# Performance work log

Measured on AMD Instinct MI355X. Metric: run time of the kernel, lower is better.

The kernel has to match this reference:

```python
import jax, jax.numpy as jnp
import numpy as np

B, N, C = 8192, 4, 768          # B = batch*tokens, N = n_streams, C = dim
HID = 4 * C                      # FFN hidden
EPS_RMS = 1.1920929e-7           # torch.finfo(float32).eps (nn.RMSNorm default eps=None)
EPS_SK = 1e-6                    # sinkhorn eps
SK_ITERS = 20
ALPHA = 0.01


def setup_inputs() -> dict:
    key = jax.random.key(0)
    ks = jax.random.split(key, 7)
    w = lambda k, shape: (jax.random.normal(k, shape, jnp.float32) * 0.02)
    return {
        "x": jax.random.normal(ks[0], (B, N, C), jnp.float32),
        "norm_w": jnp.ones((N * C,), jnp.float32),
        "w_pre": w(ks[1], (N, N * C)),
        "b_pre": jnp.zeros((N,), jnp.float32),
        "w_post": w(ks[2], (N, N * C)),
        "b_post": jnp.zeros((N,), jnp.float32),
        "w_res": w(ks[3], (N * N, N * C)),
        "b_res": jnp.zeros((N * N,), jnp.float32),
        "alpha_pre": jnp.array(ALPHA, jnp.float32),
        "alpha_post": jnp.array(ALPHA, jnp.float32),
        "alpha_res": jnp.array(ALPHA, jnp.float32),
        "w1": w(ks[4], (HID, C)),   # torch Linear weight layout [out, in]
        "b1": jnp.zeros((HID,), jnp.float32),
        "w2": w(ks[5], (C, HID)),
        "b2": jnp.zeros((C,), jnp.float32),
    }


def sinkhorn_knopp(logits):
    # logits: [B, n, n] -> doubly-stochastic matrix via 20 row/col normalizations
    M0 = jnp.exp(logits)

    def body(_, M):
        M = M / (M.sum(axis=-1, keepdims=True) + EPS_SK)
        M = M / (M.sum(axis=-2, keepdims=True) + EPS_SK)
        return M

    return jax.lax.fori_loop(0, SK_ITERS, body, M0)


def reference(x, norm_w, w_pre, b_pre, w_post, b_post, w_res, b_res,
              alpha_pre, alpha_post, alpha_res, w1, b1, w2, b2):
    b, n, c = x.shape
    x_flat = x.reshape(b, n * c)
    # RMSNorm over flattened streams
    x_norm = x_flat * jax.lax.rsqrt(jnp.mean(x_flat * x_flat, axis=-1, keepdims=True) + EPS_RMS) * norm_w
    # gate logits
    pre = alpha_pre * (x_norm @ w_pre.T) + b_pre            # [B, n]
    post = alpha_post * (x_norm @ w_post.T) + b_post        # [B, n]
    res_logits = (alpha_res * (x_norm @ w_res.T) + b_res).reshape(b, n, n)
    H_pre = jax.nn.sigmoid(pre)
    H_post = 2.0 * jax.nn.sigmoid(post)
    H_res = sinkhorn_knopp(res_logits)                      # [B, n, n]
    # pre-gate + stream mixing
    x_pre = x * H_pre[..., None]                            # [B, n, C]
    x_streams = jnp.einsum('bij,bjc->bic', H_res, x_pre)
    # fn = FFN applied on [B*n, C]
    h = jax.nn.gelu(x_streams.reshape(b * n, c) @ w1.T + b1, approximate=False)
    y = (h @ w2.T + b2).reshape(b, n, c)
    y = y * H_post[..., None]
    # residual mixed by the same DSM
    res = jnp.einsum('bij,bjc->bic', H_res, x)
    return res + y
```

## Files before the change

### kernel.cpp

```cpp
#include <hip/hip_runtime.h>

#define EPS_RMS 1.1920929e-7f
#define EPS_SK  1e-6f

typedef __bf16 bf16;
typedef __bf16 bf16x4 __attribute__((ext_vector_type(4)));
typedef __bf16 bf16x8 __attribute__((ext_vector_type(8)));
typedef float  f32x4  __attribute__((ext_vector_type(4)));

typedef __attribute__((address_space(3))) void lds_void;
typedef __attribute__((address_space(1))) void glb_void;

__device__ __forceinline__ void async_copy16(void* lds_dst, const void* gsrc) {
  __builtin_amdgcn_global_load_lds((glb_void*)gsrc, (lds_void*)lds_dst, 16, 0, 0);
}

template<int N> __device__ __forceinline__ void wait_vmcnt() {
  if constexpr (N == 6)      asm volatile("s_waitcnt vmcnt(6)" ::: "memory");
  else if constexpr (N == 5) asm volatile("s_waitcnt vmcnt(5)" ::: "memory");
  else                       asm volatile("s_waitcnt vmcnt(0)" ::: "memory");
}
__device__ __forceinline__ void lgkm0_fence() {
  asm volatile("s_waitcnt lgkmcnt(0)" ::: "memory");
  __builtin_amdgcn_sched_barrier(0);
}

__device__ __forceinline__ void xcd_swizzle(int& bx, int& by) {
  const int gx = gridDim.x, nwg = gx * gridDim.y;
  const int flat = blockIdx.y * gx + blockIdx.x;
  const int q = nwg >> 3, r = nwg & 7;
  const int xcd = flat & 7, i = flat >> 3;
  const int lin = (xcd < r ? xcd * (q + 1) : r * (q + 1) + (xcd - r) * q) + i;
  bx = lin % gx;
  by = lin / gx;
}

__global__ __launch_bounds__(256) void convert_w_kernel(
    const float* __restrict__ w1, const float* __restrict__ w2,
    bf16* __restrict__ w1b, bf16* __restrict__ w2b) {
  size_t i = ((size_t)blockIdx.x * 256 + threadIdx.x) * 4;
  f32x4 a = *(const f32x4*)(w1 + i);
  f32x4 b = *(const f32x4*)(w2 + i);
  bf16x4 ab, bb;
#pragma unroll
  for (int q = 0; q < 4; ++q) { ab[q] = (bf16)a[q]; bb[q] = (bf16)b[q]; }
  *(bf16x4*)(w1b + i) = ab;
  *(bf16x4*)(w2b + i) = bb;
}

__global__ __launch_bounds__(256) void prep_wnb_kernel(
    const float* __restrict__ w_pre, const float* __restrict__ w_post,
    const float* __restrict__ w_res, const float* __restrict__ norm_w,
    bf16* __restrict__ wnb) {
  const int i = (blockIdx.x * 256 + threadIdx.x) * 4;
  const int j = i / 3072, k = i - j * 3072;
  f32x4 wv;
  if (j < 24) {
    const float* src = j < 4 ? (w_pre + j * 3072)
                     : (j < 8 ? (w_post + (j - 4) * 3072) : (w_res + (j - 8) * 3072));
    const f32x4 nv = *(const f32x4*)(norm_w + k);
    wv = *(const f32x4*)(src + k);
    wv = wv * nv;
  } else {
    wv = f32x4{0.f, 0.f, 0.f, 0.f};
  }
  bf16x4 o;
#pragma unroll
  for (int q = 0; q < 4; ++q) o[q] = (bf16)wv[q];
  *(bf16x4*)(wnb + i) = o;
}

__global__ __launch_bounds__(256) void gates_kernel(
    const float* __restrict__ x, const bf16* __restrict__ wnb,
    const float* __restrict__ b_pre, const float* __restrict__ b_post,
    const float* __restrict__ b_res,
    const float* __restrict__ alpha_pre, const float* __restrict__ alpha_post,
    const float* __restrict__ alpha_res, float* __restrict__ gates) {
  const int t = threadIdx.x, wv = t >> 6, l = t & 63;
  const int r0 = blockIdx.x * 16;
  __shared__ float buf[4][16][32];
  __shared__ float bsq[4][16];

  f32x4 acc[2] = {};
  float sq = 0.f;
  const int kbase = wv * 768;
  const size_t arow = (size_t)(r0 + (l & 15)) * 3072;
  const int koff = (l >> 4) * 8;
#pragma unroll 1
  for (int ks = 0; ks < 24; ++ks) {
    const int k0 = kbase + ks * 32 + koff;
    const f32x4 a0 = *(const f32x4*)(x + arow + k0);
    const f32x4 a1 = *(const f32x4*)(x + arow + k0 + 4);
    sq += a0[0]*a0[0] + a0[1]*a0[1] + a0[2]*a0[2] + a0[3]*a0[3]
        + a1[0]*a1[0] + a1[1]*a1[1] + a1[2]*a1[2] + a1[3]*a1[3];
    bf16x8 af;
#pragma unroll
    for (int e = 0; e < 4; ++e) { af[e] = (bf16)a0[e]; af[4 + e] = (bf16)a1[e]; }
#pragma unroll
    for (int nf = 0; nf < 2; ++nf) {
      const bf16x8 bn = *(const bf16x8*)(wnb + (size_t)(nf * 16 + (l & 15)) * 3072 + k0);
      acc[nf] = __builtin_amdgcn_mfma_f32_16x16x32_bf16(af, bn, acc[nf], 0, 0, 0);
    }
  }
  sq += __shfl_xor(sq, 16);
  sq += __shfl_xor(sq, 32);
#pragma unroll
  for (int nf = 0; nf < 2; ++nf)
#pragma unroll
    for (int j = 0; j < 4; ++j)
      buf[wv][(l >> 4) * 4 + j][nf * 16 + (l & 15)] = acc[nf][j];
  if (l < 16) bsq[wv][l] = sq;
  __syncthreads();

  if (t < 16) {
    const int r = t;
    float dv[24];
#pragma unroll
    for (int j = 0; j < 24; ++j)
      dv[j] = buf[0][r][j] + buf[1][r][j] + buf[2][r][j] + buf[3][r][j];
    const float ssq = bsq[0][r] + bsq[1][r] + bsq[2][r] + bsq[3][r];
    const float rms = rsqrtf(ssq * (1.f / 3072.f) + EPS_RMS);
    const float ap = alpha_pre[0], apo = alpha_post[0], ar = alpha_res[0];
    float* g = gates + (size_t)(r0 + r) * 24;
    float M[16];
#pragma unroll
    for (int j = 0; j < 4; ++j) {
      const float p = ap * rms * dv[j] + b_pre[j];
      g[j] = 1.f / (1.f + __expf(-p));
      const float q = apo * rms * dv[4 + j] + b_post[j];
      g[4 + j] = 2.f / (1.f + __expf(-q));
    }
#pragma unroll
    for (int j = 0; j < 16; ++j) M[j] = __expf(ar * rms * dv[8 + j] + b_res[j]);
    for (int it = 0; it < 20; ++it) {
#pragma unroll
      for (int i = 0; i < 4; ++i) {
        const float s = M[i * 4] + M[i * 4 + 1] + M[i * 4 + 2] + M[i * 4 + 3] + EPS_SK;
        const float ri = __fdividef(1.f, s);
#pragma unroll
        for (int j = 0; j < 4; ++j) M[i * 4 + j] *= ri;
      }
#pragma unroll
      for (int j = 0; j < 4; ++j) {
        const float s = M[j] + M[4 + j] + M[8 + j] + M[12 + j] + EPS_SK;
        const float ri = __fdividef(1.f, s);
#pragma unroll
        for (int i = 0; i < 4; ++i) M[i * 4 + j] *= ri;
      }
    }
#pragma unroll
    for (int j = 0; j < 16; ++j) g[8 + j] = M[j];
  }
}

__global__ __launch_bounds__(256) void mix_kernel(
    const float* __restrict__ x, const float* __restrict__ gates,
    bf16* __restrict__ xs, bf16* __restrict__ resb) {
  const int t = threadIdx.x;
  const int b = blockIdx.x * 4 + (t >> 6);
  const int lane = t & 63;
  const float* g = gates + (size_t)b * 24;
  float mr[4][4], mp[4][4];
#pragma unroll
  for (int i = 0; i < 4; ++i)
#pragma unroll
    for (int j = 0; j < 4; ++j) {
      mr[i][j] = g[8 + i * 4 + j];
      mp[i][j] = mr[i][j] * g[j];
    }
#pragma unroll
  for (int cc = 0; cc < 3; ++cc) {
    const int c4 = lane + cc * 64;
    f32x4 xj[4];
#pragma unroll
    for (int j = 0; j < 4; ++j)
      xj[j] = *(const f32x4*)(x + (size_t)(b * 4 + j) * 768 + c4 * 4);
#pragma unroll
    for (int i = 0; i < 4; ++i) {
      f32x4 vr = mr[i][0] * xj[0] + mr[i][1] * xj[1] + mr[i][2] * xj[2] + mr[i][3] * xj[3];
      f32x4 vs = mp[i][0] * xj[0] + mp[i][1] * xj[1] + mp[i][2] * xj[2] + mp[i][3] * xj[3];
      bf16x4 ro, so;
#pragma unroll
      for (int qq = 0; qq < 4; ++qq) { ro[qq] = (bf16)vr[qq]; so[qq] = (bf16)vs[qq]; }
      *(bf16x4*)(resb + (size_t)(b * 4 + i) * 768 + c4 * 4) = ro;
      *(bf16x4*)(xs   + (size_t)(b * 4 + i) * 768 + c4 * 4) = so;
    }
  }
}

__device__ __forceinline__ void stage_block(
    const bf16* __restrict__ src, const int rowBase, const int K, const int k0,
    char* ldsBuf, const int blk, const int t) {
  const int r = t >> 3;
  const int c = (t & 7) ^ (r & 7);
  async_copy16(ldsBuf + blk * 8192 + t * 16,
               src + (size_t)(rowBase + blk * 64 + r) * K + k0 + c * 8);
}

template<int NB>
__device__ __forceinline__ void gemm256_core(
    const bf16* __restrict__ A, const bf16* __restrict__ B, const int K,
    const int tM, const int tN, char* AL, char* BL, f32x4 (&acc)[8][NB]) {
  constexpr int BBUF = NB * 8192;
  constexpr int NB1 = 2, NB2 = NB - 2;
  const int t = threadIdx.x, l = t & 63, w = t >> 6;
  const int wr = w >> 2, wc = w & 3;
  const int NT = K >> 6;
  const int arow = wr * 128 + (l & 15);
  const int brow = wc * (NB * 16) + (l & 15);
  const int cb = l >> 4;

  auto frag = [&](const char* base, int row, int ks) -> bf16x8 {
    const int c = ks * 4 + cb;
    return *(const bf16x8*)(base + row * 128 + ((c ^ (row & 7)) << 4));
  };

#pragma unroll
  for (int b = 0; b < 4; ++b) stage_block(A, tM, K, 0, AL, b, t);
#pragma unroll
  for (int b = 0; b < NB; ++b) stage_block(B, tN, K, 0, BL, b, t);
  stage_block(A, tM, K, 64, AL + 32768, 0, t);
  stage_block(A, tM, K, 64, AL + 32768, 2, t);
#pragma unroll
  for (int b = 0; b < NB; ++b) stage_block(B, tN, K, 64, BL + BBUF, b, t);
  wait_vmcnt<NB + 2>();
  __builtin_amdgcn_s_barrier();

  for (int T = 0; T < NT; ++T) {
    char* Ab = AL + (T & 1) * 32768;
    char* Bb = BL + (T & 1) * BBUF;
    char* An = AL + ((T + 1) & 1) * 32768;
    const int k1 = (T + 1) << 6, k2 = (T + 2) << 6;
    const bool s1 = (T + 1 < NT), s2 = (T + 2 < NT);
    bf16x8 af[4][2], b0[NB1][2], b1[NB2][2];

#pragma unroll
    for (int ks = 0; ks < 2; ++ks) {
#pragma unroll
      for (int ni = 0; ni < NB1; ++ni) b0[ni][ks] = frag(Bb, brow + ni * 16, ks);
#pragma unroll
      for (int mi = 0; mi < 4; ++mi) af[mi][ks] = frag(Ab, arow + mi * 16, ks);
    }
    __builtin_amdgcn_s_barrier();
    if (s1) { stage_block(A, tM, K, k1, An, 1, t); stage_block(A, tM, K, k1, An, 3, t); }
    lgkm0_fence();
    __builtin_amdgcn_s_setprio(1);
#pragma unroll
    for (int ks = 0; ks < 2; ++ks)
#pragma unroll
      for (int mi = 0; mi < 4; ++mi)
#pragma unroll
        for (int ni = 0; ni < NB1; ++ni)
          acc[mi][ni] = __builtin_amdgcn_mfma_f32_16x16x32_bf16(af[mi][ks], b0[ni][ks], acc[mi][ni], 0, 0, 0);
    __builtin_amdgcn_s_setprio(0);

#pragma unroll
    for (int ks = 0; ks < 2; ++ks)
#pragma unroll
      for (int ni = 0; ni < NB2; ++ni) b1[ni][ks] = frag(Bb, brow + (NB1 + ni) * 16, ks);
    __builtin_amdgcn_s_barrier();
    if (s2) { stage_block(A, tM, K, k2, Ab, 0, t); stage_block(A, tM, K, k2, Ab, 2, t); }
    lgkm0_fence();
    __builtin_amdgcn_s_setprio(1);
#pragma unroll
    for (int ks = 0; ks < 2; ++ks)
#pragma unroll
      for (int mi = 0; mi < 4; ++mi)
#pragma unroll
        for (int ni = 0; ni < NB2; ++ni)
          acc[mi][NB1 + ni] = __builtin_amdgcn_mfma_f32_16x16x32_bf16(af[mi][ks], b1[ni][ks], acc[mi][NB1 + ni], 0, 0, 0);
    __builtin_amdgcn_s_setprio(0);

#pragma unroll
    for (int ks = 0; ks < 2; ++ks)
#pragma unroll
      for (int mi = 0; mi < 4; ++mi) af[mi][ks] = frag(Ab, arow + (4 + mi) * 16, ks);
    __builtin_amdgcn_s_barrier();
    if (s2) { stage_block(B, tN, K, k2, Bb, 0, t); stage_block(B, tN, K, k2, Bb, 1, t); }
    lgkm0_fence();
    __builtin_amdgcn_s_setprio(1);
#pragma unroll
    for (int ks = 0; ks < 2; ++ks)
#pragma unroll
      for (int mi = 0; mi < 4; ++mi)
#pragma unroll
        for (int ni = 0; ni < NB1; ++ni)
          acc[4 + mi][ni] = __builtin_amdgcn_mfma_f32_16x16x32_bf16(af[mi][ks], b0[ni][ks], acc[4 + mi][ni], 0, 0, 0);
    __builtin_amdgcn_s_setprio(0);

    __builtin_amdgcn_s_barrier();
    if (s2) {
#pragma unroll
      for (int b = 2; b < NB; ++b) stage_block(B, tN, K, k2, Bb, b, t);
    }
    if (T < NT - 2)       wait_vmcnt<NB + 2>();
    else if (T == NT - 2) wait_vmcnt<0>();
    __builtin_amdgcn_s_setprio(1);
#pragma unroll
    for (int ks = 0; ks < 2; ++ks)
#pragma unroll
      for (int mi = 0; mi < 4; ++mi)
#pragma unroll
        for (int ni = 0; ni < NB2; ++ni)
          acc[4 + mi][NB1 + ni] = __builtin_amdgcn_mfma_f32_16x16x32_bf16(af[mi][ks], b1[ni][ks], acc[4 + mi][NB1 + ni], 0, 0, 0);
    __builtin_amdgcn_s_setprio(0);
  }
}

__global__ __launch_bounds__(512, 1) void ffn1_kernel(
    const bf16* __restrict__ xs, const bf16* __restrict__ w1b,
    const float* __restrict__ b1, bf16* __restrict__ h) {
  __shared__ __align__(16) char AL[2 * 32768];
  __shared__ __align__(16) char BL[2 * 32768];
  int bx, by; xcd_swizzle(bx, by);
  const int tM = by * 256, tN = bx * 256;
  f32x4 acc[8][4] = {};
  gemm256_core<4>(xs, w1b, 768, tM, tN, AL, BL, acc);

  const int t = threadIdx.x, l = t & 63;
  const int w = t >> 6, wr = w >> 2, wc = w & 3;
  float bias[4];
#pragma unroll
  for (int ni = 0; ni < 4; ++ni) bias[ni] = b1[tN + wc * 64 + ni * 16 + (l & 15)];
#pragma unroll
  for (int mi = 0; mi < 8; ++mi)
#pragma unroll
    for (int j = 0; j < 4; ++j) {
      const int m = tM + wr * 128 + mi * 16 + (l >> 4) * 4 + j;
#pragma unroll
      for (int ni = 0; ni < 4; ++ni) {
        const int n = tN + wc * 64 + ni * 16 + (l & 15);
        const float v = acc[mi][ni][j] + bias[ni];
        const float y2 = 1.5957691216f * (v + 0.044715f * v * v * v);
        const float g = __fdividef(v, 1.f + __expf(-y2));
        h[(size_t)m * 3072 + n] = (bf16)g;
      }
    }
}

__global__ __launch_bounds__(512, 1) void ffn2_kernel(
    const bf16* __restrict__ h, const bf16* __restrict__ w2b,
    const float* __restrict__ b2, const float* __restrict__ gates,
    const bf16* __restrict__ resb, float* __restrict__ outp, const int m0) {
  __shared__ __align__(16) char AL[2 * 32768];
  __shared__ __align__(16) char BL[2 * 24576];
  int bx, by; xcd_swizzle(bx, by);
  const int tM = by * 256, tN = bx * 192;
  f32x4 acc[8][3] = {};
  gemm256_core<3>(h, w2b, 3072, tM, tN, AL, BL, acc);

  const int t = threadIdx.x, l = t & 63;
  const int w = t >> 6, wr = w >> 2, wc = w & 3;
  float bias[3];
#pragma unroll
  for (int ni = 0; ni < 3; ++ni) bias[ni] = b2[tN + wc * 48 + ni * 16 + (l & 15)];
#pragma unroll
  for (int mi = 0; mi < 8; ++mi)
#pragma unroll
    for (int j = 0; j < 4; ++j) {
      const int mL = tM + wr * 128 + mi * 16 + (l >> 4) * 4 + j;
      const int mG = m0 + mL;
      const float hp = gates[(size_t)(mG >> 2) * 24 + 4 + (mG & 3)];
#pragma unroll
      for (int ni = 0; ni < 3; ++ni) {
        const int n = tN + wc * 48 + ni * 16 + (l & 15);
        const size_t o = (size_t)mG * 768 + n;
        outp[o] = (float)resb[o] + (acc[mi][ni][j] + bias[ni]) * hp;
      }
    }
}

extern "C" void kernel_launch(void* const* d_in, const int* in_sizes, int n_in,
                              void* d_out, int out_size, void* d_ws, size_t ws_size,
                              hipStream_t stream) {
  (void)in_sizes; (void)n_in; (void)out_size;
  const float* x         = (const float*)d_in[0];
  const float* norm_w    = (const float*)d_in[1];
  const float* w_pre     = (const float*)d_in[2];
  const float* b_pre     = (const float*)d_in[3];
  const float* w_post    = (const float*)d_in[4];
  const float* b_post    = (const float*)d_in[5];
  const float* w_res     = (const float*)d_in[6];
  const float* b_res     = (const float*)d_in[7];
  const float* alpha_pre = (const float*)d_in[8];
  const float* alpha_post= (const float*)d_in[9];
  const float* alpha_res = (const float*)d_in[10];
  const float* w1        = (const float*)d_in[11];
  const float* b1        = (const float*)d_in[12];
  const float* w2        = (const float*)d_in[13];
  const float* b2        = (const float*)d_in[14];
  float* outp = (float*)d_out;

  char* ws = (char*)d_ws;
  float* gates = (float*)ws;
  bf16*  w1b   = (bf16*)(ws + 786432);
  bf16*  w2b   = (bf16*)(ws + 5505024);
  bf16*  xs    = (bf16*)(ws + 10223616);
  bf16*  resb  = (bf16*)(ws + 60555264);
  bf16*  wnb   = (bf16*)(ws + 110886912);
  bf16*  h     = (bf16*)(ws + 111083520);

  size_t avail = ws_size > 111083520 ? ws_size - 111083520 : 0;
  long hrows = (long)(avail / (3072 * 2));
  hrows = (hrows / 256) * 256;
  if (hrows > 32768) hrows = 32768;
  if (hrows < 256) hrows = 256;

  convert_w_kernel<<<dim3(2304), dim3(256), 0, stream>>>(w1, w2, w1b, w2b);
  prep_wnb_kernel<<<dim3(96), dim3(256), 0, stream>>>(w_pre, w_post, w_res, norm_w, wnb);
  gates_kernel<<<dim3(512), dim3(256), 0, stream>>>(
      x, wnb, b_pre, b_post, b_res, alpha_pre, alpha_post, alpha_res, gates);
  mix_kernel<<<dim3(2048), dim3(256), 0, stream>>>(x, gates, xs, resb);

  for (long mo = 0; mo < 32768; mo += hrows) {
    const long mm = (32768 - mo) < hrows ? (32768 - mo) : hrows;
    ffn1_kernel<<<dim3(12, (unsigned)(mm / 256)), dim3(512), 0, stream>>>(
        xs + mo * 768, w1b, b1, h);
    ffn2_kernel<<<dim3(4, (unsigned)(mm / 256)), dim3(512), 0, stream>>>(
        h, w2b, b2, gates, resb, outp, (int)mo);
  }
}
```

Measured before the change: 484.3 us.

## Fuse stream mixing into gates kernel and simplify GEMM inner pipeline

Merges the separate mix kernel into the gates kernel. The sinkhorn matrix and pre-gate go through shared memory and the same block writes xs and resb, so one launch and the gates round-trip disappear. The x rows are re-read while likely still in cache. The GEMM core is also restructured from four B-fragment phases into two half-M phases, with all B fragments loaded up front and all next-tile staging issued at one point. This raises register pressure for B fragments and reduces the interleaving of loads with MFMA.

```diff
diff --git a/kernel.cpp b/kernel.cpp
--- a/kernel.cpp
+++ b/kernel.cpp
@@ -75,11 +75,13 @@
     const float* __restrict__ b_pre, const float* __restrict__ b_post,
     const float* __restrict__ b_res,
     const float* __restrict__ alpha_pre, const float* __restrict__ alpha_post,
-    const float* __restrict__ alpha_res, float* __restrict__ gates) {
+    const float* __restrict__ alpha_res, float* __restrict__ gates,
+    bf16* __restrict__ xs, bf16* __restrict__ resb) {
   const int t = threadIdx.x, wv = t >> 6, l = t & 63;
   const int r0 = blockIdx.x * 16;
   __shared__ float buf[4][16][32];
   __shared__ float bsq[4][16];
+  __shared__ float gm[16][20];
 
   f32x4 acc[2] = {};
   float sq = 0.f;
@@ -123,10 +125,12 @@
     const float ap = alpha_pre[0], apo = alpha_post[0], ar = alpha_res[0];
     float* g = gates + (size_t)(r0 + r) * 24;
     float M[16];
+    float hp[4];
 #pragma unroll
     for (int j = 0; j < 4; ++j) {
       const float p = ap * rms * dv[j] + b_pre[j];
-      g[j] = 1.f / (1.f + __expf(-p));
+      hp[j] = 1.f / (1.f + __expf(-p));
+      g[j] = hp[j];
       const float q = apo * rms * dv[4 + j] + b_post[j];
       g[4 + j] = 2.f / (1.f + __expf(-q));
     }
@@ -149,41 +153,38 @@
       }
     }
 #pragma unroll
-    for (int j = 0; j < 16; ++j) g[8 + j] = M[j];
-  }
-}
-
-__global__ __launch_bounds__(256) void mix_kernel(
-    const float* __restrict__ x, const float* __restrict__ gates,
-    bf16* __restrict__ xs, bf16* __restrict__ resb) {
-  const int t = threadIdx.x;
-  const int b = blockIdx.x * 4 + (t >> 6);
-  const int lane = t & 63;
-  const float* g = gates + (size_t)b * 24;
+    for (int j = 0; j < 16; ++j) { g[8 + j] = M[j]; gm[r][j] = M[j]; }
+#pragma unroll
+    for (int j = 0; j < 4; ++j) gm[r][16 + j] = hp[j];
+  }
+  __syncthreads();
+
+  const int bb = t >> 4, tt = t & 15;
   float mr[4][4], mp[4][4];
 #pragma unroll
   for (int i = 0; i < 4; ++i)
 #pragma unroll
     for (int j = 0; j < 4; ++j) {
-      mr[i][j] = g[8 + i * 4 + j];
-      mp[i][j] = mr[i][j] * g[j];
-    }
-#pragma unroll
-  for (int cc = 0; cc < 3; ++cc) {
-    const int c4 = lane + cc * 64;
+      mr[i][j] = gm[bb][i * 4 + j];
+      mp[i][j] = mr[i][j] * gm[bb][16 + j];
+    }
+  const size_t xb = (size_t)(r0 + bb) * 3072;
+#pragma unroll 1
+  for (int cc = 0; cc < 12; ++cc) {
+    const int c4 = (tt + cc * 16) * 4;
     f32x4 xj[4];
 #pragma unroll
     for (int j = 0; j < 4; ++j)
-      xj[j] = *(const f32x4*)(x + (size_t)(b * 4 + j) * 768 + c4 * 4);
+      xj[j] = *(const f32x4*)(x + xb + (size_t)j * 768 + c4);
 #pragma unroll
     for (int i = 0; i < 4; ++i) {
       f32x4 vr = mr[i][0] * xj[0] + mr[i][1] * xj[1] + mr[i][2] * xj[2] + mr[i][3] * xj[3];
       f32x4 vs = mp[i][0] * xj[0] + mp[i][1] * xj[1] + mp[i][2] * xj[2] + mp[i][3] * xj[3];
       bf16x4 ro, so;
 #pragma unroll
-      for (int qq = 0; qq < 4; ++qq) { ro[qq] = (bf16)vr[qq]; so[qq] = (bf16)vs[qq]; }
-      *(bf16x4*)(resb + (size_t)(b * 4 + i) * 768 + c4 * 4) = ro;
-      *(bf16x4*)(xs   + (size_t)(b * 4 + i) * 768 + c4 * 4) = so;
+      for (int q = 0; q < 4; ++q) { ro[q] = (bf16)vr[q]; so[q] = (bf16)vs[q]; }
+      *(bf16x4*)(resb + xb + (size_t)i * 768 + c4) = ro;
+      *(bf16x4*)(xs   + xb + (size_t)i * 768 + c4) = so;
     }
   }
 }
@@ -202,7 +203,6 @@
     const bf16* __restrict__ A, const bf16* __restrict__ B, const int K,
     const int tM, const int tN, char* AL, char* BL, f32x4 (&acc)[8][NB]) {
   constexpr int BBUF = NB * 8192;
-  constexpr int NB1 = 2, NB2 = NB - 2;
   const int t = threadIdx.x, l = t & 63, w = t >> 6;
   const int wr = w >> 2, wc = w & 3;
   const int NT = K >> 6;
@@ -232,12 +232,12 @@
     char* An = AL + ((T + 1) & 1) * 32768;
     const int k1 = (T + 1) << 6, k2 = (T + 2) << 6;
     const bool s1 = (T + 1 < NT), s2 = (T + 2 < NT);
-    bf16x8 af[4][2], b0[NB1][2], b1[NB2][2];
+    bf16x8 af[4][2], bfv[NB][2];
 
 #pragma unroll
     for (int ks = 0; ks < 2; ++ks) {
 #pragma unroll
-      for (int ni = 0; ni < NB1; ++ni) b0[ni][ks] = frag(Bb, brow + ni * 16, ks);
+      for (int ni = 0; ni < NB; ++ni) bfv[ni][ks] = frag(Bb, brow + ni * 16, ks);
 #pragma unroll
       for (int mi = 0; mi < 4; ++mi) af[mi][ks] = frag(Ab, arow + mi * 16, ks);
     }
@@ -250,16 +250,22 @@
 #pragma unroll
       for (int mi = 0; mi < 4; ++mi)
 #pragma unroll
-        for (int ni = 0; ni < NB1; ++ni)
-          acc[mi][ni] = __builtin_amdgcn_mfma_f32_16x16x32_bf16(af[mi][ks], b0[ni][ks], acc[mi][ni], 0, 0, 0);
+        for (int ni = 0; ni < NB; ++ni)
+          acc[mi][ni] = __builtin_amdgcn_mfma_f32_16x16x32_bf16(af[mi][ks], bfv[ni][ks], acc[mi][ni], 0, 0, 0);
     __builtin_amdgcn_s_setprio(0);
 
 #pragma unroll
     for (int ks = 0; ks < 2; ++ks)
 #pragma unroll
-      for (int ni = 0; ni < NB2; ++ni) b1[ni][ks] = frag(Bb, brow + (NB1 + ni) * 16, ks);
+      for (int mi = 0; mi < 4; ++mi) af[mi][ks] = frag(Ab, arow + (4 + mi) * 16, ks);
     __builtin_amdgcn_s_barrier();
-    if (s2) { stage_block(A, tM, K, k2, Ab, 0, t); stage_block(A, tM, K, k2, Ab, 2, t); }
+    if (s2) {
+      stage_block(A, tM, K, k2, Ab, 0, t); stage_block(A, tM, K, k2, Ab, 2, t);
+#pragma unroll
+      for (int b = 0; b < NB; ++b) stage_block(B, tN, K, k2, Bb, b, t);
+    }
+    if (T < NT - 2)       wait_vmcnt<NB + 2>();
+    else if (T == NT - 2) wait_vmcnt<0>();
     lgkm0_fence();
     __builtin_amdgcn_s_setprio(1);
 #pragma unroll
@@ -267,42 +273,8 @@
 #pragma unroll
       for (int mi = 0; mi < 4; ++mi)
 #pragma unroll
-        for (int ni = 0; ni < NB2; ++ni)
-          acc[mi][NB1 + ni] = __builtin_amdgcn_mfma_f32_16x16x32_bf16(af[mi][ks], b1[ni][ks], acc[mi][NB1 + ni], 0, 0, 0);
-    __builtin_amdgcn_s_setprio(0);
-
-#pragma unroll
-    for (int ks = 0; ks < 2; ++ks)
-#pragma unroll
-      for (int mi = 0; mi < 4; ++mi) af[mi][ks] = frag(Ab, arow + (4 + mi) * 16, ks);
-    __builtin_amdgcn_s_barrier();
-    if (s2) { stage_block(B, tN, K, k2, Bb, 0, t); stage_block(B, tN, K, k2, Bb, 1, t); }
-    lgkm0_fence();
-    __builtin_amdgcn_s_setprio(1);
-#pragma unroll
-    for (int ks = 0; ks < 2; ++ks)
-#pragma unroll
-      for (int mi = 0; mi < 4; ++mi)
-#pragma unroll
-        for (int ni = 0; ni < NB1; ++ni)
-          acc[4 + mi][ni] = __builtin_amdgcn_mfma_f32_16x16x32_bf16(af[mi][ks], b0[ni][ks], acc[4 + mi][ni], 0, 0, 0);
-    __builtin_amdgcn_s_setprio(0);
-
-    __builtin_amdgcn_s_barrier();
-    if (s2) {
-#pragma unroll
-      for (int b = 2; b < NB; ++b) stage_block(B, tN, K, k2, Bb, b, t);
-    }
-    if (T < NT - 2)       wait_vmcnt<NB + 2>();
-    else if (T == NT - 2) wait_vmcnt<0>();
-    __builtin_amdgcn_s_setprio(1);
-#pragma unroll
-    for (int ks = 0; ks < 2; ++ks)
-#pragma unroll
-      for (int mi = 0; mi < 4; ++mi)
-#pragma unroll
-        for (int ni = 0; ni < NB2; ++ni)
-          acc[4 + mi][NB1 + ni] = __builtin_amdgcn_mfma_f32_16x16x32_bf16(af[mi][ks], b1[ni][ks], acc[4 + mi][NB1 + ni], 0, 0, 0);
+        for (int ni = 0; ni < NB; ++ni)
+          acc[4 + mi][ni] = __builtin_amdgcn_mfma_f32_16x16x32_bf16(af[mi][ks], bfv[ni][ks], acc[4 + mi][ni], 0, 0, 0);
     __builtin_amdgcn_s_setprio(0);
   }
 }
@@ -409,8 +381,7 @@
   convert_w_kernel<<<dim3(2304), dim3(256), 0, stream>>>(w1, w2, w1b, w2b);
   prep_wnb_kernel<<<dim3(96), dim3(256), 0, stream>>>(w_pre, w_post, w_res, norm_w, wnb);
   gates_kernel<<<dim3(512), dim3(256), 0, stream>>>(
-      x, wnb, b_pre, b_post, b_res, alpha_pre, alpha_post, alpha_res, gates);
-  mix_kernel<<<dim3(2048), dim3(256), 0, stream>>>(x, gates, xs, resb);
+      x, wnb, b_pre, b_post, b_res, alpha_pre, alpha_post, alpha_res, gates, xs, resb);
 
   for (long mo = 0; mo < 32768; mo += hrows) {
     const long mm = (32768 - mo) < hrows ? (32768 - mo) : hrows;
```

Measured after the change: 482.0 us. No clear change (-0.5%).
